# Kernel optimization log

Measured on AMD Instinct MI355X. Metric: run time of the kernel, lower is better.

## Reference

```python
import jax, jax.numpy as jnp
import numpy as np

N = 30000      # nodes
E = 480000     # edges (before self loops)
NFEAT = 128
H = 16         # heads
C = 32         # per-head channels = nhid
NCLASS = 10
G = 64         # graphs in batch
ATT_SLOPE = 0.2   # GATv2Conv negative_slope default
ACT_SLOPE = 0.01  # F.leaky_relu default


def setup_inputs() -> dict:
    key = jax.random.key(0)
    ks = jax.random.split(key, 16)
    def glorot(k, shape):
        fan = sum(shape[:2]) if len(shape) > 1 else shape[0]
        return jax.random.normal(k, shape, jnp.float32) * (2.0 / fan) ** 0.5
    inp = {
        "x": jax.random.normal(ks[0], (N, NFEAT), jnp.float32),
        # layer 1: lin_l / lin_r map NFEAT -> H*C, attention vector att [H, C]
        "Wl1": glorot(ks[1], (NFEAT, H * C)), "bl1": jnp.zeros((H * C,), jnp.float32),
        "Wr1": glorot(ks[2], (NFEAT, H * C)), "br1": jnp.zeros((H * C,), jnp.float32),
        "att1": glorot(ks[3], (H, C)), "b1": jnp.zeros((C,), jnp.float32),
        # layer 2: nhid(=C) -> H*C
        "Wl2": glorot(ks[4], (C, H * C)), "bl2": jnp.zeros((H * C,), jnp.float32),
        "Wr2": glorot(ks[5], (C, H * C)), "br2": jnp.zeros((H * C,), jnp.float32),
        "att2": glorot(ks[6], (H, C)), "b2": jnp.zeros((C,), jnp.float32),
        # classifier nhid -> nclass
        "Wc": glorot(ks[7], (C, NCLASS)), "bc": jnp.zeros((NCLASS,), jnp.float32),
        "edge_index": jax.random.randint(ks[8], (2, E), 0, N, jnp.int32),
        "batch": jnp.sort(jax.random.randint(ks[9], (N,), 0, G, jnp.int32)),
    }
    return inp


def _gatv2_layer(x, Wl, bl, Wr, br, att, b, src, dst, n):
    # GATv2Conv, concat=False (mean over heads), eval mode (no dropout)
    xl = (x @ Wl + bl).reshape(n, H, C)   # messages (x_j)
    xr = (x @ Wr + br).reshape(n, H, C)   # query side (x_i)
    e = jax.nn.leaky_relu(xl[src] + xr[dst], ATT_SLOPE)      # [E', H, C]
    score = jnp.einsum('ehc,hc->eh', e, att)                 # [E', H]
    # segment softmax over incoming edges of each dst node
    m = jax.ops.segment_max(score, dst, num_segments=n)
    ex = jnp.exp(score - m[dst])
    denom = jax.ops.segment_sum(ex, dst, num_segments=n)
    alpha = ex / denom[dst]                                  # [E', H]
    out = jax.ops.segment_sum(alpha[:, :, None] * xl[src], dst, num_segments=n)
    return out.mean(axis=1) + b                              # [n, C]


def reference(x, Wl1, bl1, Wr1, br1, att1, b1, Wl2, bl2, Wr2, br2, att2, b2, Wc, bc, edge_index, batch):
    # add self loops (PyG GATv2Conv default add_self_loops=True)
    loop = jnp.arange(N, dtype=edge_index.dtype)
    src = jnp.concatenate([edge_index[0], loop])
    dst = jnp.concatenate([edge_index[1], loop])

    h = jax.nn.leaky_relu(_gatv2_layer(x, Wl1, bl1, Wr1, br1, att1, b1, src, dst, N), ACT_SLOPE)
    h = jax.nn.leaky_relu(_gatv2_layer(h, Wl2, bl2, Wr2, br2, att2, b2, src, dst, N), ACT_SLOPE)
    # dropout is identity in eval mode
    # global mean pool over graphs
    summed = jax.ops.segment_sum(h, batch, num_segments=G)               # [G, C]
    counts = jax.ops.segment_sum(jnp.ones((N,), h.dtype), batch, num_segments=G)
    pooled = summed / jnp.maximum(counts, 1.0)[:, None]
    logits = pooled @ Wc + bc
    return logits / 1.0  # temperature = 1.0
```

## Files before the change

### kernel.cpp

```cpp
#include <hip/hip_runtime.h>
#include <float.h>

#define NNODES 30000
#define NEDGES 480000
#define NFEATK 128
#define NH 16
#define NC 32
#define HC 512
#define NCLASSES 10
#define NG 64
#define CAP 96

#define MBP 472
#define GEMM_BLOCKS (MBP * 8)
#define SCAT_BLOCKS 1875

using half4 = __attribute__((ext_vector_type(4))) _Float16;
using half8 = __attribute__((ext_vector_type(8))) _Float16;
using f32x4 = __attribute__((ext_vector_type(4))) float;

__global__ void wconv_kernel(const float* __restrict__ Wl1, const float* __restrict__ Wr1,
                             const float* __restrict__ Wl2, const float* __restrict__ Wr2,
                             _Float16* __restrict__ Wlt1, _Float16* __restrict__ Wrt1,
                             _Float16* __restrict__ Wlt2, _Float16* __restrict__ Wrt2) {
    int gtid = blockIdx.x * blockDim.x + threadIdx.x;
    int gstride = gridDim.x * blockDim.x;
    for (int i = gtid; i < 2 * 512 * NFEATK; i += gstride) {
        int sel = i >= 512 * NFEATK;
        int idx = i - sel * 512 * NFEATK;
        const float* W = sel ? Wr1 : Wl1;
        _Float16* Wt = sel ? Wrt1 : Wlt1;
        int n = idx & 511, k = idx >> 9;
        Wt[n * NFEATK + k] = (_Float16)W[idx];
    }
    for (int i = gtid; i < 2 * 512 * NC; i += gstride) {
        int sel = i >= 512 * NC;
        int idx = i - sel * 512 * NC;
        const float* W = sel ? Wr2 : Wl2;
        _Float16* Wt = sel ? Wrt2 : Wlt2;
        int n = idx & 511, k = idx >> 9;
        Wt[n * NC + k] = (_Float16)W[idx];
    }
}

template <int K, bool CONVA, bool SCATTER>
__launch_bounds__(256)
__global__ void dual_gemm_kernel(const void* __restrict__ Avoid,
                                 const _Float16* __restrict__ Wlt, const _Float16* __restrict__ Wrt,
                                 const float* __restrict__ bl, const float* __restrict__ br,
                                 _Float16* __restrict__ Yl, _Float16* __restrict__ Yr,
                                 const int* __restrict__ src, const int* __restrict__ dst,
                                 int* __restrict__ cnt, int* __restrict__ csr) {
    constexpr int Kc = K / 8;
    constexpr int AH = 64 * K;
    constexpr int BH = 128 * K;
    constexpr int YSH = 64 * 136;
    constexpr int SMEMH = (AH + BH > YSH) ? (AH + BH) : YSH;
    __shared__ __align__(16) _Float16 smem[SMEMH];
    _Float16* as = smem;
    _Float16* bs = smem + AH;

    int bid = blockIdx.x, tid = threadIdx.x;
    if constexpr (SCATTER) {
        if (bid >= GEMM_BLOCKS) {
            int e = (bid - GEMM_BLOCKS) * 256 + tid;
            if (e < NEDGES) {
                int s = src[e], d = dst[e];
                int pos = atomicAdd(&cnt[d], 1);
                csr[d * CAP + pos] = s;
            }
            return;
        }
    }
    int mb = bid % MBP;
    int yy = bid / MBP;
    if (mb * 64 >= NNODES) return;
    int sel = yy >> 2;
    int nbase = (yy & 3) * 128;
    const _Float16* Bt = sel ? Wrt : Wlt;
    const float* bias = sel ? br : bl;
    _Float16* Y = sel ? Yr : Yl;

    for (int c = tid; c < 64 * Kc; c += 256) {
        int row = c / Kc, k8 = c % Kc;
        int arow = mb * 64 + row; if (arow > NNODES - 1) arow = NNODES - 1;
        half8 v;
        if constexpr (CONVA) {
            const float* xp = (const float*)Avoid + (size_t)arow * K + k8 * 8;
            float4 f0 = *(const float4*)xp;
            float4 f1 = *(const float4*)(xp + 4);
            v = half8{(_Float16)f0.x, (_Float16)f0.y, (_Float16)f0.z, (_Float16)f0.w,
                      (_Float16)f1.x, (_Float16)f1.y, (_Float16)f1.z, (_Float16)f1.w};
        } else {
            v = *(const half8*)((const _Float16*)Avoid + (size_t)arow * K + k8 * 8);
        }
        *(half8*)&as[(row * Kc + (k8 ^ (row & (Kc - 1)))) * 8] = v;
    }
    for (int c = tid; c < 128 * Kc; c += 256) {
        int row = c / Kc, k8 = c % Kc;
        half8 v = *(const half8*)&Bt[(size_t)(nbase + row) * K + k8 * 8];
        *(half8*)&bs[(row * Kc + (k8 ^ (row & (Kc - 1)))) * 8] = v;
    }
    __syncthreads();

    int wave = tid >> 6, lane = tid & 63;
    int quad = lane >> 4, l16 = lane & 15;
    int am = l16 & (Kc - 1);

    f32x4 acc[8];
    #pragma unroll
    for (int f = 0; f < 8; f++) acc[f] = (f32x4){0.f, 0.f, 0.f, 0.f};

    #pragma unroll
    for (int kk = 0; kk < Kc; kk += 4) {
        int k8 = (kk + quad) ^ am;
        half8 a = *(const half8*)&as[((wave * 16 + l16) * Kc + k8) * 8];
        #pragma unroll
        for (int f = 0; f < 8; f++) {
            half8 b = *(const half8*)&bs[((f * 16 + l16) * Kc + k8) * 8];
            acc[f] = __builtin_amdgcn_mfma_f32_16x16x32_f16(a, b, acc[f], 0, 0, 0);
        }
    }
    __syncthreads();

    _Float16* ys = smem;
    #pragma unroll
    for (int f = 0; f < 8; f++) {
        float bv = bias[nbase + f * 16 + l16];
        #pragma unroll
        for (int r = 0; r < 4; r++) {
            ys[(wave * 16 + quad * 4 + r) * 136 + f * 16 + l16] = (_Float16)(acc[f][r] + bv);
        }
    }
    __syncthreads();
    int mtop = mb * 64;
    for (int c = tid; c < 64 * 16; c += 256) {
        int r = c >> 4, cc = (c & 15) * 8;
        int grow = mtop + r;
        if (grow < NNODES)
            *(half8*)&Y[(size_t)grow * HC + nbase + cc] = *(half8*)&ys[r * 136 + cc];
    }
}

template <typename OUT>
__launch_bounds__(128)
__global__ void gat_edge_kernel(const _Float16* __restrict__ xlh, const _Float16* __restrict__ xrh,
                                const float* __restrict__ att, const float* __restrict__ bvec,
                                const int* __restrict__ cnt, const int* __restrict__ csr_src,
                                OUT* __restrict__ hout) {
    int d = blockIdx.x;
    int t = threadIdx.x;
    int col = t * 4;
    half4 xrq = *(const half4*)&xrh[(size_t)d * HC + col];
    float4 xrv = {(float)xrq.x, (float)xrq.y, (float)xrq.z, (float)xrq.w};
    float4 attv = *(const float4*)&att[col];
    int beg = d * CAP, end = beg + cnt[d];

    float l, a0, a1, a2, a3;
    {
        half4 q = *(const half4*)&xlh[(size_t)d * HC + col];
        float x0 = (float)q.x, x1 = (float)q.y, x2 = (float)q.z, x3 = (float)q.w;
        float e, v;
        e = x0 + xrv.x; e = (e > 0.f) ? e : 0.2f * e; v  = e * attv.x;
        e = x1 + xrv.y; e = (e > 0.f) ? e : 0.2f * e; v += e * attv.y;
        e = x2 + xrv.z; e = (e > 0.f) ? e : 0.2f * e; v += e * attv.z;
        e = x3 + xrv.w; e = (e > 0.f) ? e : 0.2f * e; v += e * attv.w;
        #pragma unroll
        for (int off = 1; off < 8; off <<= 1) v += __shfl_xor(v, off);
        float p = __expf(v);
        l = p; a0 = p * x0; a1 = p * x1; a2 = p * x2; a3 = p * x3;
    }

    for (int i = beg; i < end; i += 4) {
        int n = end - i;
        int s0 = csr_src[i];
        int s1 = csr_src[n > 1 ? i + 1 : i];
        int s2 = csr_src[n > 2 ? i + 2 : i];
        int s3 = csr_src[n > 3 ? i + 3 : i];
        half4 q0 = *(const half4*)&xlh[(size_t)s0 * HC + col];
        half4 q1 = *(const half4*)&xlh[(size_t)s1 * HC + col];
        half4 q2 = *(const half4*)&xlh[(size_t)s2 * HC + col];
        half4 q3 = *(const half4*)&xlh[(size_t)s3 * HC + col];
        float x00 = (float)q0.x, x01 = (float)q0.y, x02 = (float)q0.z, x03 = (float)q0.w;
        float x10 = (float)q1.x, x11 = (float)q1.y, x12 = (float)q1.z, x13 = (float)q1.w;
        float x20 = (float)q2.x, x21 = (float)q2.y, x22 = (float)q2.z, x23 = (float)q2.w;
        float x30 = (float)q3.x, x31 = (float)q3.y, x32 = (float)q3.z, x33 = (float)q3.w;

        float e, v0, v1, v2, v3;
        e = x00 + xrv.x; e = (e > 0.f) ? e : 0.2f * e; v0  = e * attv.x;
        e = x01 + xrv.y; e = (e > 0.f) ? e : 0.2f * e; v0 += e * attv.y;
        e = x02 + xrv.z; e = (e > 0.f) ? e : 0.2f * e; v0 += e * attv.z;
        e = x03 + xrv.w; e = (e > 0.f) ? e : 0.2f * e; v0 += e * attv.w;
        e = x10 + xrv.x; e = (e > 0.f) ? e : 0.2f * e; v1  = e * attv.x;
        e = x11 + xrv.y; e = (e > 0.f) ? e : 0.2f * e; v1 += e * attv.y;
        e = x12 + xrv.z; e = (e > 0.f) ? e : 0.2f * e; v1 += e * attv.z;
        e = x13 + xrv.w; e = (e > 0.f) ? e : 0.2f * e; v1 += e * attv.w;
        e = x20 + xrv.x; e = (e > 0.f) ? e : 0.2f * e; v2  = e * attv.x;
        e = x21 + xrv.y; e = (e > 0.f) ? e : 0.2f * e; v2 += e * attv.y;
        e = x22 + xrv.z; e = (e > 0.f) ? e : 0.2f * e; v2 += e * attv.z;
        e = x23 + xrv.w; e = (e > 0.f) ? e : 0.2f * e; v2 += e * attv.w;
        e = x30 + xrv.x; e = (e > 0.f) ? e : 0.2f * e; v3  = e * attv.x;
        e = x31 + xrv.y; e = (e > 0.f) ? e : 0.2f * e; v3 += e * attv.y;
        e = x32 + xrv.z; e = (e > 0.f) ? e : 0.2f * e; v3 += e * attv.z;
        e = x33 + xrv.w; e = (e > 0.f) ? e : 0.2f * e; v3 += e * attv.w;

        #pragma unroll
        for (int off = 1; off < 8; off <<= 1) {
            v0 += __shfl_xor(v0, off);
            v1 += __shfl_xor(v1, off);
            v2 += __shfl_xor(v2, off);
            v3 += __shfl_xor(v3, off);
        }
        float p0 = __expf(v0);
        float p1 = (n > 1) ? __expf(v1) : 0.f;
        float p2 = (n > 2) ? __expf(v2) : 0.f;
        float p3 = (n > 3) ? __expf(v3) : 0.f;
        l += (p0 + p1) + (p2 + p3);
        a0 += p0 * x00 + p1 * x10 + p2 * x20 + p3 * x30;
        a1 += p0 * x01 + p1 * x11 + p2 * x21 + p3 * x31;
        a2 += p0 * x02 + p1 * x12 + p2 * x22 + p3 * x32;
        a3 += p0 * x03 + p1 * x13 + p2 * x23 + p3 * x33;
    }
    float inv = 1.0f / l;
    float4 o = {a0 * inv, a1 * inv, a2 * inv, a3 * inv};

    __shared__ float red[512];
    *(float4*)&red[col] = o;
    __syncthreads();
    if (t < 32) {
        float ssum = 0.f;
        #pragma unroll
        for (int hh = 0; hh < NH; ++hh) ssum += red[hh * 32 + t];
        float r = ssum * (1.0f / (float)NH) + bvec[t];
        r = (r > 0.f) ? r : 0.01f * r;
        hout[d * NC + t] = (OUT)r;
    }
}

__launch_bounds__(1024)
__global__ void pool_classify_kernel(const float* __restrict__ h, const int* __restrict__ batch,
                                     const float* __restrict__ Wc, const float* __restrict__ bc,
                                     float* __restrict__ out) {
    int g = blockIdx.x;
    int lo = 0, hi = NNODES;
    while (lo < hi) { int mid = (lo + hi) >> 1; if (batch[mid] < g) lo = mid + 1; else hi = mid; }
    int start = lo;
    hi = NNODES;
    while (lo < hi) { int mid = (lo + hi) >> 1; if (batch[mid] <= g) lo = mid + 1; else hi = mid; }
    int endn = lo;
    int cntg = endn - start;

    int tid = threadIdx.x;
    int c = tid & 31, nl = tid >> 5;
    float s = 0.f;
    for (int n = start + nl; n < endn; n += 32) s += h[n * NC + c];
    __shared__ float red[1024];
    red[tid] = s;
    __syncthreads();
    if (tid < 32) {
        float t = 0.f;
        #pragma unroll
        for (int j = 0; j < 32; j++) t += red[j * 32 + tid];
        red[tid] = t / fmaxf((float)cntg, 1.0f);
    }
    __syncthreads();
    if (tid < NCLASSES) {
        float sum = bc[tid];
        #pragma unroll
        for (int cc = 0; cc < NC; cc++) sum += red[cc] * Wc[cc * NCLASSES + tid];
        out[g * NCLASSES + tid] = sum;
    }
}


extern "C" void kernel_launch(void* const* d_in, const int* in_sizes, int n_in,
                              void* d_out, int out_size, void* d_ws, size_t ws_size,
                              hipStream_t stream) {
    const float* x    = (const float*)d_in[0];
    const float* Wl1  = (const float*)d_in[1];
    const float* bl1  = (const float*)d_in[2];
    const float* Wr1  = (const float*)d_in[3];
    const float* br1  = (const float*)d_in[4];
    const float* att1 = (const float*)d_in[5];
    const float* b1   = (const float*)d_in[6];
    const float* Wl2  = (const float*)d_in[7];
    const float* bl2  = (const float*)d_in[8];
    const float* Wr2  = (const float*)d_in[9];
    const float* br2  = (const float*)d_in[10];
    const float* att2 = (const float*)d_in[11];
    const float* b2   = (const float*)d_in[12];
    const float* Wc   = (const float*)d_in[13];
    const float* bc   = (const float*)d_in[14];
    const int* ei     = (const int*)d_in[15];
    const int* batch  = (const int*)d_in[16];
    float* out = (float*)d_out;

    const int* srcp = ei;
    const int* dstp = ei + NEDGES;

    char* ws = (char*)d_ws;
    size_t off = 0;
    auto alloc = [&](size_t bytes) -> void* {
        void* p = ws + off;
        off += (bytes + 255) & ~(size_t)255;
        return p;
    };
    _Float16* xlh  = (_Float16*)alloc(sizeof(_Float16) * (size_t)NNODES * HC);
    _Float16* xrh  = (_Float16*)alloc(sizeof(_Float16) * (size_t)NNODES * HC);
    _Float16* h1   = (_Float16*)alloc(sizeof(_Float16) * (size_t)NNODES * NC);
    float* h2      = (float*)alloc(sizeof(float) * (size_t)NNODES * NC);
    _Float16* Wlt1 = (_Float16*)alloc(sizeof(_Float16) * 512 * NFEATK);
    _Float16* Wrt1 = (_Float16*)alloc(sizeof(_Float16) * 512 * NFEATK);
    _Float16* Wlt2 = (_Float16*)alloc(sizeof(_Float16) * 512 * NC);
    _Float16* Wrt2 = (_Float16*)alloc(sizeof(_Float16) * 512 * NC);
    int*   cnt     = (int*)alloc(sizeof(int) * NNODES);
    int*   csr     = (int*)alloc(sizeof(int) * (size_t)NNODES * CAP);

    hipMemsetAsync(cnt, 0, sizeof(int) * NNODES, stream);

    wconv_kernel<<<320, 256, 0, stream>>>(Wl1, Wr1, Wl2, Wr2, Wlt1, Wrt1, Wlt2, Wrt2);

    dual_gemm_kernel<NFEATK, true, true><<<GEMM_BLOCKS + SCAT_BLOCKS, 256, 0, stream>>>(
        x, Wlt1, Wrt1, bl1, br1, xlh, xrh, srcp, dstp, cnt, csr);
    gat_edge_kernel<_Float16><<<NNODES, 128, 0, stream>>>(xlh, xrh, att1, b1, cnt, csr, h1);

    dual_gemm_kernel<NC, false, false><<<GEMM_BLOCKS, 256, 0, stream>>>(
        h1, Wlt2, Wrt2, bl2, br2, xlh, xrh, nullptr, nullptr, nullptr, nullptr);
    gat_edge_kernel<float><<<NNODES, 128, 0, stream>>>(xlh, xrh, att2, b2, cnt, csr, h2);

    pool_classify_kernel<<<NG, 1024, 0, stream>>>(h2, batch, Wc, bc, out);
}
```

Baseline: 324.1 us.

## Process one destination node per wavefront with 8-wide half loads in GAT edge kernel

The edge aggregation kernel now assigns one 64-lane wavefront per destination node, two nodes per 128-thread block. Each lane handles 8 channels through half8 loads, so the per-head score reduction needs only two shuffles instead of three. The memset of the count array is folded into the weight-conversion kernel, removing one separate operation. Per-lane register use rises, and each wavefront now serialises over its node's edges with twice as many channels per lane.

```diff
diff --git a/kernel.cpp b/kernel.cpp
--- a/kernel.cpp
+++ b/kernel.cpp
@@ -22,9 +22,11 @@
 __global__ void wconv_kernel(const float* __restrict__ Wl1, const float* __restrict__ Wr1,
                              const float* __restrict__ Wl2, const float* __restrict__ Wr2,
                              _Float16* __restrict__ Wlt1, _Float16* __restrict__ Wrt1,
-                             _Float16* __restrict__ Wlt2, _Float16* __restrict__ Wrt2) {
+                             _Float16* __restrict__ Wlt2, _Float16* __restrict__ Wrt2,
+                             int* __restrict__ cnt) {
     int gtid = blockIdx.x * blockDim.x + threadIdx.x;
     int gstride = gridDim.x * blockDim.x;
+    for (int i = gtid; i < NNODES; i += gstride) cnt[i] = 0;
     for (int i = gtid; i < 2 * 512 * NFEATK; i += gstride) {
         int sel = i >= 512 * NFEATK;
         int idx = i - sel * 512 * NFEATK;
@@ -148,27 +150,41 @@
                                 const float* __restrict__ att, const float* __restrict__ bvec,
                                 const int* __restrict__ cnt, const int* __restrict__ csr_src,
                                 OUT* __restrict__ hout) {
-    int d = blockIdx.x;
-    int t = threadIdx.x;
-    int col = t * 4;
-    half4 xrq = *(const half4*)&xrh[(size_t)d * HC + col];
-    float4 xrv = {(float)xrq.x, (float)xrq.y, (float)xrq.z, (float)xrq.w};
-    float4 attv = *(const float4*)&att[col];
+    __shared__ float red[2][512];
+    int w = threadIdx.x >> 6, lane = threadIdx.x & 63;
+    int d = blockIdx.x * 2 + w;
+    int col = lane * 8;
+
+    half8 xrq = *(const half8*)&xrh[(size_t)d * HC + col];
+    float4 at0 = *(const float4*)&att[col];
+    float4 at1 = *(const float4*)&att[col + 4];
+    float xr[8], at[8];
+    #pragma unroll
+    for (int c = 0; c < 8; c++) xr[c] = (float)xrq[c];
+    at[0] = at0.x; at[1] = at0.y; at[2] = at0.z; at[3] = at0.w;
+    at[4] = at1.x; at[5] = at1.y; at[6] = at1.z; at[7] = at1.w;
+
     int beg = d * CAP, end = beg + cnt[d];
 
-    float l, a0, a1, a2, a3;
+    float l, acc[8];
     {
-        half4 q = *(const half4*)&xlh[(size_t)d * HC + col];
-        float x0 = (float)q.x, x1 = (float)q.y, x2 = (float)q.z, x3 = (float)q.w;
-        float e, v;
-        e = x0 + xrv.x; e = (e > 0.f) ? e : 0.2f * e; v  = e * attv.x;
-        e = x1 + xrv.y; e = (e > 0.f) ? e : 0.2f * e; v += e * attv.y;
-        e = x2 + xrv.z; e = (e > 0.f) ? e : 0.2f * e; v += e * attv.z;
-        e = x3 + xrv.w; e = (e > 0.f) ? e : 0.2f * e; v += e * attv.w;
-        #pragma unroll
-        for (int off = 1; off < 8; off <<= 1) v += __shfl_xor(v, off);
+        half8 q = *(const half8*)&xlh[(size_t)d * HC + col];
+        float xv[8];
+        #pragma unroll
+        for (int c = 0; c < 8; c++) xv[c] = (float)q[c];
+        float v = 0.f;
+        #pragma unroll
+        for (int c = 0; c < 8; c++) {
+            float e = xv[c] + xr[c];
+            e = (e > 0.f) ? e : 0.2f * e;
+            v += e * at[c];
+        }
+        v += __shfl_xor(v, 1);
+        v += __shfl_xor(v, 2);
         float p = __expf(v);
-        l = p; a0 = p * x0; a1 = p * x1; a2 = p * x2; a3 = p * x3;
+        l = p;
+        #pragma unroll
+        for (int c = 0; c < 8; c++) acc[c] = p * xv[c];
     }
 
     for (int i = beg; i < end; i += 4) {
@@ -177,63 +193,53 @@
         int s1 = csr_src[n > 1 ? i + 1 : i];
         int s2 = csr_src[n > 2 ? i + 2 : i];
         int s3 = csr_src[n > 3 ? i + 3 : i];
-        half4 q0 = *(const half4*)&xlh[(size_t)s0 * HC + col];
-        half4 q1 = *(const half4*)&xlh[(size_t)s1 * HC + col];
-        half4 q2 = *(const half4*)&xlh[(size_t)s2 * HC + col];
-        half4 q3 = *(const half4*)&xlh[(size_t)s3 * HC + col];
-        float x00 = (float)q0.x, x01 = (float)q0.y, x02 = (float)q0.z, x03 = (float)q0.w;
-        float x10 = (float)q1.x, x11 = (float)q1.y, x12 = (float)q1.z, x13 = (float)q1.w;
-        float x20 = (float)q2.x, x21 = (float)q2.y, x22 = (float)q2.z, x23 = (float)q2.w;
-        float x30 = (float)q3.x, x31 = (float)q3.y, x32 = (float)q3.z, x33 = (float)q3.w;
-
-        float e, v0, v1, v2, v3;
-        e = x00 + xrv.x; e = (e > 0.f) ? e : 0.2f * e; v0  = e * attv.x;
-        e = x01 + xrv.y; e = (e > 0.f) ? e : 0.2f * e; v0 += e * attv.y;
-        e = x02 + xrv.z; e = (e > 0.f) ? e : 0.2f * e; v0 += e * attv.z;
-        e = x03 + xrv.w; e = (e > 0.f) ? e : 0.2f * e; v0 += e * attv.w;
-        e = x10 + xrv.x; e = (e > 0.f) ? e : 0.2f * e; v1  = e * attv.x;
-        e = x11 + xrv.y; e = (e > 0.f) ? e : 0.2f * e; v1 += e * attv.y;
-        e = x12 + xrv.z; e = (e > 0.f) ? e : 0.2f * e; v1 += e * attv.z;
-        e = x13 + xrv.w; e = (e > 0.f) ? e : 0.2f * e; v1 += e * attv.w;
-        e = x20 + xrv.x; e = (e > 0.f) ? e : 0.2f * e; v2  = e * attv.x;
-        e = x21 + xrv.y; e = (e > 0.f) ? e : 0.2f * e; v2 += e * attv.y;
-        e = x22 + xrv.z; e = (e > 0.f) ? e : 0.2f * e; v2 += e * attv.z;
-        e = x23 + xrv.w; e = (e > 0.f) ? e : 0.2f * e; v2 += e * attv.w;
-        e = x30 + xrv.x; e = (e > 0.f) ? e : 0.2f * e; v3  = e * attv.x;
-        e = x31 + xrv.y; e = (e > 0.f) ? e : 0.2f * e; v3 += e * attv.y;
-        e = x32 + xrv.z; e = (e > 0.f) ? e : 0.2f * e; v3 += e * attv.z;
-        e = x33 + xrv.w; e = (e > 0.f) ? e : 0.2f * e; v3 += e * attv.w;
-
-        #pragma unroll
-        for (int off = 1; off < 8; off <<= 1) {
-            v0 += __shfl_xor(v0, off);
-            v1 += __shfl_xor(v1, off);
-            v2 += __shfl_xor(v2, off);
-            v3 += __shfl_xor(v3, off);
-        }
+        half8 q0 = *(const half8*)&xlh[(size_t)s0 * HC + col];
+        half8 q1 = *(const half8*)&xlh[(size_t)s1 * HC + col];
+        half8 q2 = *(const half8*)&xlh[(size_t)s2 * HC + col];
+        half8 q3 = *(const half8*)&xlh[(size_t)s3 * HC + col];
+        float xv[4][8];
+        #pragma unroll
+        for (int c = 0; c < 8; c++) {
+            xv[0][c] = (float)q0[c];
+            xv[1][c] = (float)q1[c];
+            xv[2][c] = (float)q2[c];
+            xv[3][c] = (float)q3[c];
+        }
+        float v0 = 0.f, v1 = 0.f, v2 = 0.f, v3 = 0.f;
+        #pragma unroll
+        for (int c = 0; c < 8; c++) {
+            float e;
+            e = xv[0][c] + xr[c]; e = (e > 0.f) ? e : 0.2f * e; v0 += e * at[c];
+            e = xv[1][c] + xr[c]; e = (e > 0.f) ? e : 0.2f * e; v1 += e * at[c];
+            e = xv[2][c] + xr[c]; e = (e > 0.f) ? e : 0.2f * e; v2 += e * at[c];
+            e = xv[3][c] + xr[c]; e = (e > 0.f) ? e : 0.2f * e; v3 += e * at[c];
+        }
+        v0 += __shfl_xor(v0, 1); v1 += __shfl_xor(v1, 1);
+        v2 += __shfl_xor(v2, 1); v3 += __shfl_xor(v3, 1);
+        v0 += __shfl_xor(v0, 2); v1 += __shfl_xor(v1, 2);
+        v2 += __shfl_xor(v2, 2); v3 += __shfl_xor(v3, 2);
         float p0 = __expf(v0);
         float p1 = (n > 1) ? __expf(v1) : 0.f;
         float p2 = (n > 2) ? __expf(v2) : 0.f;
         float p3 = (n > 3) ? __expf(v3) : 0.f;
         l += (p0 + p1) + (p2 + p3);
-        a0 += p0 * x00 + p1 * x10 + p2 * x20 + p3 * x30;
-        a1 += p0 * x01 + p1 * x11 + p2 * x21 + p3 * x31;
-        a2 += p0 * x02 + p1 * x12 + p2 * x22 + p3 * x32;
-        a3 += p0 * x03 + p1 * x13 + p2 * x23 + p3 * x33;
+        #pragma unroll
+        for (int c = 0; c < 8; c++) {
+            acc[c] += p0 * xv[0][c] + p1 * xv[1][c];
+            acc[c] += p2 * xv[2][c] + p3 * xv[3][c];
+        }
     }
     float inv = 1.0f / l;
-    float4 o = {a0 * inv, a1 * inv, a2 * inv, a3 * inv};
-
-    __shared__ float red[512];
-    *(float4*)&red[col] = o;
-    __syncthreads();
-    if (t < 32) {
-        float ssum = 0.f;
-        #pragma unroll
-        for (int hh = 0; hh < NH; ++hh) ssum += red[hh * 32 + t];
-        float r = ssum * (1.0f / (float)NH) + bvec[t];
+    #pragma unroll
+    for (int c = 0; c < 8; c++) red[w][col + c] = acc[c] * inv;
+    __syncthreads();
+    if (lane < 32) {
+        float s = 0.f;
+        #pragma unroll
+        for (int hh = 0; hh < NH; ++hh) s += red[w][hh * 32 + lane];
+        float r = s * (1.0f / (float)NH) + bvec[lane];
         r = (r > 0.f) ? r : 0.01f * r;
-        hout[d * NC + t] = (OUT)r;
+        hout[d * NC + lane] = (OUT)r;
     }
 }
 
@@ -316,17 +322,15 @@
     int*   cnt     = (int*)alloc(sizeof(int) * NNODES);
     int*   csr     = (int*)alloc(sizeof(int) * (size_t)NNODES * CAP);
 
-    hipMemsetAsync(cnt, 0, sizeof(int) * NNODES, stream);
-
-    wconv_kernel<<<320, 256, 0, stream>>>(Wl1, Wr1, Wl2, Wr2, Wlt1, Wrt1, Wlt2, Wrt2);
+    wconv_kernel<<<320, 256, 0, stream>>>(Wl1, Wr1, Wl2, Wr2, Wlt1, Wrt1, Wlt2, Wrt2, cnt);
 
     dual_gemm_kernel<NFEATK, true, true><<<GEMM_BLOCKS + SCAT_BLOCKS, 256, 0, stream>>>(
         x, Wlt1, Wrt1, bl1, br1, xlh, xrh, srcp, dstp, cnt, csr);
-    gat_edge_kernel<_Float16><<<NNODES, 128, 0, stream>>>(xlh, xrh, att1, b1, cnt, csr, h1);
+    gat_edge_kernel<_Float16><<<NNODES / 2, 128, 0, stream>>>(xlh, xrh, att1, b1, cnt, csr, h1);
 
     dual_gemm_kernel<NC, false, false><<<GEMM_BLOCKS, 256, 0, stream>>>(
         h1, Wlt2, Wrt2, bl2, br2, xlh, xrh, nullptr, nullptr, nullptr, nullptr);
-    gat_edge_kernel<float><<<NNODES, 128, 0, stream>>>(xlh, xrh, att2, b2, cnt, csr, h2);
+    gat_edge_kernel<float><<<NNODES / 2, 128, 0, stream>>>(xlh, xrh, att2, b2, cnt, csr, h2);
 
     pool_classify_kernel<<<NG, 1024, 0, stream>>>(h2, batch, Wc, bc, out);
 }
```

New measurement: 333.2 us. 1.03x slower.
